# Kernel optimization log

Measured on AMD Instinct MI355X. Metric: run time of the kernel, lower is better.

Reference implementation:

```python
import jax, jax.numpy as jnp
import numpy as np

B, S, D, DOUT, E = 2, 2048, 1024, 1024, 8
DH = 4 * D  # expert hidden size


def setup_inputs() -> dict:
    key = jax.random.key(0)
    ks = jax.random.split(key, 7)
    sc = lambda *sh: 1.0 / np.sqrt(sh[-2]) if len(sh) >= 2 else 0.02
    return {
        "x": jax.random.normal(ks[0], (B, S, D), jnp.float32),
        "Wg": jax.random.normal(ks[1], (D, E), jnp.float32) / np.sqrt(D),
        "bg": jnp.zeros((E,), jnp.float32),
        "W1": jax.random.normal(ks[2], (E, D, DH), jnp.float32) / np.sqrt(D),
        "b1": jax.random.normal(ks[3], (E, DH), jnp.float32) * 0.02,
        "W2": jax.random.normal(ks[4], (E, DH, DOUT), jnp.float32) / np.sqrt(DH),
        "b2": jax.random.normal(ks[5], (E, DOUT), jnp.float32) * 0.02,
    }


def reference(x, Wg, bg, W1, b1, W2, b2):
    # x: [B, S, D] -> flatten tokens (chunking over seq in the original is
    # math-neutral: routing and expert MLP are per-token).
    Bb, Ss, Dd = x.shape
    xt = x.reshape(-1, Dd)                       # [T, D]
    # Gate: softmax then argmax (top-1 routing, output NOT scaled by gate prob)
    gates = jax.nn.softmax(xt @ Wg + bg, axis=-1)  # [T, E]
    sel = jnp.argmax(gates, axis=-1)               # [T]
    nE = W1.shape[0]
    out = jnp.zeros((xt.shape[0], W2.shape[-1]), x.dtype)
    # Grouped expert MLP expressed as masked dense loop over the small fixed
    # expert count (jit-friendly; a fused gather-grouped-GEMM-scatter kernel
    # is the optimization target).
    for e in range(nE):
        h = jax.nn.gelu(xt @ W1[e] + b1[e], approximate=False)  # [T, 4D]
        ye = h @ W2[e] + b2[e]                                  # [T, DOUT]
        out = jnp.where((sel == e)[:, None], ye, out)
    return out.reshape(Bb, Ss, -1)
```

## Files before the change

### kernel.cpp

```cpp
#include <hip/hip_runtime.h>
#include <hip/hip_bf16.h>
#include <math.h>

#define T_TOK 4096
#define DIM   1024
#define NEXP  8
#define DHID  4096
#define NDOUT 1024
#define BM    128
#define MAXTILES 40

typedef short bf16x8 __attribute__((ext_vector_type(8)));
typedef float f32x4 __attribute__((ext_vector_type(4)));

__device__ __forceinline__ unsigned short f2bf(float f) {
  unsigned u = __float_as_uint(f);
  u += 0x7fffu + ((u >> 16) & 1u);
  return (unsigned short)(u >> 16);
}
__device__ __forceinline__ unsigned pack2bf(float a, float b) {
  return (unsigned)f2bf(a) | ((unsigned)f2bf(b) << 16);
}
__device__ __forceinline__ void gl_lds16(const void* g, void* l) {
  __builtin_amdgcn_global_load_lds(
      (const __attribute__((address_space(1))) void*)g,
      (__attribute__((address_space(3))) void*)l, 16, 0, 0);
}
#define SBAR()  __builtin_amdgcn_s_barrier()
#define SCHED() __builtin_amdgcn_sched_barrier(0)

__global__ __launch_bounds__(256)
void gate_kernel(const float* __restrict__ x, const float* __restrict__ Wg,
                 const float* __restrict__ bg, int* __restrict__ sel,
                 unsigned short* __restrict__ xbf) {
  int lane = threadIdx.x & 63;
  int wid  = threadIdx.x >> 6;
  int t = blockIdx.x * 4 + wid;
  if (t >= T_TOK) return;
  const float* xr = x + (size_t)t * DIM;
  unsigned short* xbr = xbf + (size_t)t * DIM;
  double acc[NEXP];
#pragma unroll
  for (int e = 0; e < NEXP; e++) acc[e] = 0.0;
#pragma unroll
  for (int j = 0; j < 4; j++) {
    int d0 = j * 256 + lane * 4;
    float4 v = *(const float4*)(xr + d0);
    uint2 p; p.x = pack2bf(v.x, v.y); p.y = pack2bf(v.z, v.w);
    *(uint2*)(xbr + d0) = p;
    float xs[4] = {v.x, v.y, v.z, v.w};
#pragma unroll
    for (int i = 0; i < 4; i++) {
      const float4* wr = reinterpret_cast<const float4*>(Wg + (size_t)(d0 + i) * NEXP);
      float4 w0 = wr[0], w1 = wr[1];
      double xv = (double)xs[i];
      acc[0] += xv * (double)w0.x;
      acc[1] += xv * (double)w0.y;
      acc[2] += xv * (double)w0.z;
      acc[3] += xv * (double)w0.w;
      acc[4] += xv * (double)w1.x;
      acc[5] += xv * (double)w1.y;
      acc[6] += xv * (double)w1.z;
      acc[7] += xv * (double)w1.w;
    }
  }
#pragma unroll
  for (int off = 32; off >= 1; off >>= 1) {
#pragma unroll
    for (int e = 0; e < NEXP; e++) acc[e] += __shfl_down(acc[e], off);
  }
  if (lane == 0) {
    double best = acc[0] + (double)bg[0];
    int bi = 0;
#pragma unroll
    for (int e = 1; e < NEXP; e++) {
      double v = acc[e] + (double)bg[e];
      if (v > best) { best = v; bi = e; }
    }
    sel[t] = bi;
  }
}

__global__ void zero_kernel(int* __restrict__ counts) {
  if (threadIdx.x < NEXP) counts[threadIdx.x] = 0;
}

__global__ void hist_kernel(const int* __restrict__ sel, int* __restrict__ counts) {
  __shared__ int lc[NEXP];
  if (threadIdx.x < NEXP) lc[threadIdx.x] = 0;
  __syncthreads();
  int t = blockIdx.x * 256 + threadIdx.x;
  atomicAdd(&lc[sel[t]], 1);
  __syncthreads();
  if (threadIdx.x < NEXP) atomicAdd(&counts[threadIdx.x], lc[threadIdx.x]);
}

__global__ void plan_kernel(const int* __restrict__ counts, int* __restrict__ base,
                            int* __restrict__ cursor, int* __restrict__ tileExpert,
                            int* __restrict__ tilePos, int* __restrict__ tileRows,
                            int* __restrict__ ntiles) {
  if (threadIdx.x == 0) {
    int acc = 0, nt = 0;
    for (int e = 0; e < NEXP; e++) {
      base[e] = acc; cursor[e] = acc;
      int c = counts[e];
      for (int j = 0; j < c; j += BM) {
        tileExpert[nt] = e;
        tilePos[nt]    = acc + j;
        int rem = c - j;
        tileRows[nt]   = rem < BM ? rem : BM;
        nt++;
      }
      acc += c;
    }
    *ntiles = nt;
  }
}

__global__ void scatter_kernel(const int* __restrict__ sel, int* __restrict__ cursor,
                               int* __restrict__ list) {
  __shared__ int lcnt[NEXP];
  __shared__ int lbase[NEXP];
  int tid = threadIdx.x;
  if (tid < NEXP) lcnt[tid] = 0;
  __syncthreads();
  int t = blockIdx.x * 256 + tid;
  int e = sel[t];
  int lpos = atomicAdd(&lcnt[e], 1);
  __syncthreads();
  if (tid < NEXP) lbase[tid] = atomicAdd(&cursor[tid], lcnt[tid]);
  __syncthreads();
  list[lbase[e] + lpos] = t;
}

__global__ __launch_bounds__(256)
void transpose_tile_kernel(const float* __restrict__ in, unsigned short* __restrict__ out,
                           int K, int N) {
  int nb = blockIdx.x, kb = blockIdx.y, e = blockIdx.z;
  const float* inp = in + (size_t)e * K * N;
  __shared__ unsigned short lds[128][72];
  int tx = threadIdx.x;
  int kloc = tx >> 5;
  int n4   = (tx & 31) << 2;
#pragma unroll
  for (int p = 0; p < 8; p++) {
    int k = p * 8 + kloc;
    float4 v = *(const float4*)(inp + (size_t)(kb * 64 + k) * N + nb * 128 + n4);
    lds[n4 + 0][k] = f2bf(v.x);
    lds[n4 + 1][k] = f2bf(v.y);
    lds[n4 + 2][k] = f2bf(v.z);
    lds[n4 + 3][k] = f2bf(v.w);
  }
  __syncthreads();
  char* tile = (char*)(out + (((size_t)e * gridDim.x + nb) * gridDim.y + kb) * 8192);
  int r  = tx >> 1;
  int kc0 = (tx & 1) * 32;
#pragma unroll
  for (int c = 0; c < 4; c++) {
    int kc = kc0 + c * 8;
    uint4 v = *(const uint4*)&lds[r][kc];
    *(uint4*)(tile + r * 128 + ((2 * kc) ^ ((r & 7) << 4))) = v;
  }
}


__global__ __launch_bounds__(256)
void gemm1_kernel(const unsigned short* __restrict__ xbf, const unsigned short* __restrict__ W1T,
                  const float* __restrict__ b1, const int* __restrict__ list,
                  const int* __restrict__ tileExpert, const int* __restrict__ tilePos,
                  const int* __restrict__ tileRows, const int* __restrict__ ntiles,
                  unsigned short* __restrict__ HcT) {
  int tIdx = blockIdx.y;
  if (tIdx >= *ntiles) return;
  int e = tileExpert[tIdx], posBase = tilePos[tIdx], rows = tileRows[tIdx];
  int nb = blockIdx.x;

  __shared__ __align__(1024) char As[2][16384];
  __shared__ __align__(1024) char Bs[2][16384];

  const int tx = threadIdx.x, lane = tx & 63, w = tx >> 6;
  const int wm = w >> 1, wn = w & 1;
  const int rsub = lane >> 3;
  const int px = ((lane & 7) ^ rsub) << 4;

  const char* aS[4];
#pragma unroll
  for (int j = 0; j < 4; j++) {
    int r = w * 32 + j * 8 + rsub;
    int tok = list[posBase + (r < rows ? r : rows - 1)];
    aS[j] = (const char*)xbf + (size_t)tok * (DIM * 2) + px;
  }
  const char* bTile = (const char*)W1T + (((size_t)e * (DHID / 128) + nb) * (DIM / 64)) * 16384
                      + w * 4096 + lane * 16;

  auto STAGE = [&](int buf, int kt) {
#pragma unroll
    for (int j = 0; j < 4; j++) {
      gl_lds16(aS[j] + kt * 128, &As[buf][(w * 32 + j * 8) * 128]);
      gl_lds16(bTile + kt * 16384 + j * 1024, &Bs[buf][w * 4096 + j * 1024]);
    }
  };

  f32x4 acc[4][4];
#pragma unroll
  for (int mf = 0; mf < 4; mf++)
#pragma unroll
    for (int nf = 0; nf < 4; nf++)
      acc[mf][nf] = f32x4{0.f, 0.f, 0.f, 0.f};

  auto COMPUTE = [&](int buf) {
#pragma unroll
    for (int ks = 0; ks < 2; ks++) {
      int koff = (ks * 64 + (lane >> 4) * 16) ^ ((lane & 7) << 4);
      bf16x8 aF[4], bF[4];
#pragma unroll
      for (int mf = 0; mf < 4; mf++)
        aF[mf] = *(const bf16x8*)&As[buf][(wm * 64 + mf * 16 + (lane & 15)) * 128 + koff];
#pragma unroll
      for (int nf = 0; nf < 4; nf++)
        bF[nf] = *(const bf16x8*)&Bs[buf][(wn * 64 + nf * 16 + (lane & 15)) * 128 + koff];
#pragma unroll
      for (int mf = 0; mf < 4; mf++)
#pragma unroll
        for (int nf = 0; nf < 4; nf++)
          acc[mf][nf] = __builtin_amdgcn_mfma_f32_16x16x32_bf16(aF[mf], bF[nf], acc[mf][nf], 0, 0, 0);
    }
  };

  const int NT = DIM / 64;
  STAGE(0, 0);
  for (int kt = 0; kt < NT; kt++) {
    int buf = kt & 1;
    if (kt + 1 < NT) {
      STAGE(buf ^ 1, kt + 1);
      asm volatile("s_waitcnt vmcnt(8)" ::: "memory");
    } else {
      asm volatile("s_waitcnt vmcnt(0)" ::: "memory");
    }
    SCHED(); SBAR(); SCHED();
    COMPUTE(buf);
    SCHED(); SBAR(); SCHED();
  }

  const float* b1e = b1 + (size_t)e * DHID;
  char* hBase = (char*)(HcT + (size_t)tIdx * (DHID / 64) * 8192);
#pragma unroll
  for (int nf = 0; nf < 4; nf++) {
    int col = nb * 128 + wn * 64 + nf * 16 + (lane & 15);
    int kt2 = col >> 6;
    int colk2 = (col & 63) * 2;
    float bias = b1e[col];
    char* tile = hBase + (size_t)kt2 * 16384;
#pragma unroll
    for (int mf = 0; mf < 4; mf++) {
#pragma unroll
      for (int j = 0; j < 4; j++) {
        int r = wm * 64 + mf * 16 + ((lane >> 4) << 2) + j;
        float h = acc[mf][nf][j] + bias;
        float g = 0.5f * h * (1.0f + erff(h * 0.70710678118654752f));
        *(unsigned short*)(tile + r * 128 + (colk2 ^ ((r & 7) << 4))) = f2bf(g);
      }
    }
  }
}

__global__ __launch_bounds__(256)
void gemm2_kernel(const unsigned short* __restrict__ HcT, const unsigned short* __restrict__ W2T,
                  const float* __restrict__ b2, const int* __restrict__ tileExpert,
                  const int* __restrict__ tilePos, const int* __restrict__ tileRows,
                  const int* __restrict__ ntiles, float* __restrict__ Ppart) {
  int tIdx = blockIdx.y;
  if (tIdx >= *ntiles) return;
  int e = tileExpert[tIdx], posBase = tilePos[tIdx], rows = tileRows[tIdx];
  int nb = blockIdx.x;
  int zs = blockIdx.z;

  __shared__ __align__(1024) char As[2][16384];
  __shared__ __align__(1024) char Bs[2][16384];

  const int tx = threadIdx.x, lane = tx & 63, w = tx >> 6;
  const int wm = w >> 1, wn = w & 1;

  const char* aTile = (const char*)HcT + (size_t)tIdx * (DHID / 64) * 16384
                      + (size_t)zs * 32 * 16384 + w * 4096 + lane * 16;
  const char* bTile = (const char*)W2T + (((size_t)e * (NDOUT / 128) + nb) * (DHID / 64)) * 16384
                      + (size_t)zs * 32 * 16384 + w * 4096 + lane * 16;

  auto STAGE = [&](int buf, int kt) {
#pragma unroll
    for (int j = 0; j < 4; j++) {
      gl_lds16(aTile + kt * 16384 + j * 1024, &As[buf][w * 4096 + j * 1024]);
      gl_lds16(bTile + kt * 16384 + j * 1024, &Bs[buf][w * 4096 + j * 1024]);
    }
  };

  f32x4 acc[4][4];
#pragma unroll
  for (int mf = 0; mf < 4; mf++)
#pragma unroll
    for (int nf = 0; nf < 4; nf++)
      acc[mf][nf] = f32x4{0.f, 0.f, 0.f, 0.f};

  auto COMPUTE = [&](int buf) {
#pragma unroll
    for (int ks = 0; ks < 2; ks++) {
      int koff = (ks * 64 + (lane >> 4) * 16) ^ ((lane & 7) << 4);
      bf16x8 aF[4], bF[4];
#pragma unroll
      for (int mf = 0; mf < 4; mf++)
        aF[mf] = *(const bf16x8*)&As[buf][(wm * 64 + mf * 16 + (lane & 15)) * 128 + koff];
#pragma unroll
      for (int nf = 0; nf < 4; nf++)
        bF[nf] = *(const bf16x8*)&Bs[buf][(wn * 64 + nf * 16 + (lane & 15)) * 128 + koff];
#pragma unroll
      for (int mf = 0; mf < 4; mf++)
#pragma unroll
        for (int nf = 0; nf < 4; nf++)
          acc[mf][nf] = __builtin_amdgcn_mfma_f32_16x16x32_bf16(aF[mf], bF[nf], acc[mf][nf], 0, 0, 0);
    }
  };

  const int NT = 32;
  STAGE(0, 0);
  for (int kt = 0; kt < NT; kt++) {
    int buf = kt & 1;
    if (kt + 1 < NT) {
      STAGE(buf ^ 1, kt + 1);
      asm volatile("s_waitcnt vmcnt(8)" ::: "memory");
    } else {
      asm volatile("s_waitcnt vmcnt(0)" ::: "memory");
    }
    SCHED(); SBAR(); SCHED();
    COMPUTE(buf);
    SCHED(); SBAR(); SCHED();
  }

  const float* b2e = b2 + (size_t)e * NDOUT;
  float* P = Ppart + (size_t)zs * T_TOK * NDOUT;
#pragma unroll
  for (int nf = 0; nf < 4; nf++) {
    int col = nb * 128 + wn * 64 + nf * 16 + (lane & 15);
    float bias = (zs == 0) ? b2e[col] : 0.f;
#pragma unroll
    for (int mf = 0; mf < 4; mf++)
#pragma unroll
      for (int j = 0; j < 4; j++) {
        int rloc = wm * 64 + mf * 16 + ((lane >> 4) << 2) + j;
        if (rloc < rows)
          P[(size_t)(posBase + rloc) * NDOUT + col] = acc[mf][nf][j] + bias;
      }
  }
}

__global__ __launch_bounds__(256)
void reduce_kernel(const float* __restrict__ Ppart, const int* __restrict__ list,
                   float* __restrict__ out) {
  int pos = blockIdx.x;
  int tok = list[pos];
  int c = threadIdx.x * 4;
  float4 a = *(const float4*)(Ppart + (size_t)pos * NDOUT + c);
  float4 b = *(const float4*)(Ppart + (size_t)T_TOK * NDOUT + (size_t)pos * NDOUT + c);
  float4 o; o.x = a.x + b.x; o.y = a.y + b.y; o.z = a.z + b.z; o.w = a.w + b.w;
  *(float4*)(out + (size_t)tok * NDOUT + c) = o;
}

extern "C" void kernel_launch(void* const* d_in, const int* in_sizes, int n_in,
                              void* d_out, int out_size, void* d_ws, size_t ws_size,
                              hipStream_t stream) {
  const float* x  = (const float*)d_in[0];
  const float* Wg = (const float*)d_in[1];
  const float* bg = (const float*)d_in[2];
  const float* W1 = (const float*)d_in[3];
  const float* b1 = (const float*)d_in[4];
  const float* W2 = (const float*)d_in[5];
  const float* b2 = (const float*)d_in[6];
  float* out = (float*)d_out;

  char* ws = (char*)d_ws;
  int* sel        = (int*)(ws);
  int* counts     = (int*)(ws + 16384);
  int* base       = (int*)(ws + 16448);
  int* cursor     = (int*)(ws + 16512);
  int* ntiles     = (int*)(ws + 16576);
  int* tileExpert = (int*)(ws + 16640);
  int* tilePos    = (int*)(ws + 16832);
  int* tileRows   = (int*)(ws + 17024);
  int* list       = (int*)(ws + 17408);

  unsigned short* xbf = (unsigned short*)(ws + (1ull << 20));
  unsigned short* HcT = (unsigned short*)(ws + (10ull << 20));
  unsigned short* W1T = (unsigned short*)(ws + (52ull << 20));
  unsigned short* W2T = (unsigned short*)(ws + (116ull << 20));
  float* Ppart        = (float*)(ws + (52ull << 20));

  gate_kernel<<<T_TOK / 4, 256, 0, stream>>>(x, Wg, bg, sel, xbf);
  zero_kernel<<<1, 64, 0, stream>>>(counts);
  hist_kernel<<<T_TOK / 256, 256, 0, stream>>>(sel, counts);
  plan_kernel<<<1, 64, 0, stream>>>(counts, base, cursor, tileExpert, tilePos, tileRows, ntiles);
  scatter_kernel<<<T_TOK / 256, 256, 0, stream>>>(sel, cursor, list);

  transpose_tile_kernel<<<dim3(DHID / 128, DIM / 64, NEXP), 256, 0, stream>>>(W1, W1T, DIM, DHID);
  transpose_tile_kernel<<<dim3(NDOUT / 128, DHID / 64, NEXP), 256, 0, stream>>>(W2, W2T, DHID, NDOUT);

  gemm1_kernel<<<dim3(DHID / 128, MAXTILES), 256, 0, stream>>>(
      xbf, W1T, b1, list, tileExpert, tilePos, tileRows, ntiles, HcT);
  gemm2_kernel<<<dim3(NDOUT / 128, MAXTILES, 2), 256, 0, stream>>>(
      HcT, W2T, b2, tileExpert, tilePos, tileRows, ntiles, Ppart);
  reduce_kernel<<<T_TOK, 256, 0, stream>>>(Ppart, list, out);
}
```

Baseline: 316.7 us.

## Single-buffer GEMM loops, tanh GELU, and LDS-staged coalesced H stores

Both expert GEMM kernels drop the double-buffered LDS prefetch with explicit vmcnt waits and use a single buffer with __syncthreads around each k-step. In GEMM1 the exact erf GELU becomes a tanh approximation built on __expf. The H tile is first written into LDS and then copied to global memory as 16-byte row stores instead of scattered 2-byte writes. Losing the prefetch means global loads no longer overlap MFMA work, and the tanh GELU changes numerics slightly.

```diff
diff --git a/kernel.cpp b/kernel.cpp
--- a/kernel.cpp
+++ b/kernel.cpp
@@ -26,8 +26,14 @@
       (const __attribute__((address_space(1))) void*)g,
       (__attribute__((address_space(3))) void*)l, 16, 0, 0);
 }
-#define SBAR()  __builtin_amdgcn_s_barrier()
-#define SCHED() __builtin_amdgcn_sched_barrier(0)
+__device__ __forceinline__ float gelu_fast(float h) {
+  float z  = 0.79788456080286536f * (h + 0.044715f * h * h * h);
+  float az = fabsf(z);
+  float et = __expf(-2.0f * az);
+  float th = (1.0f - et) / (1.0f + et);
+  th = copysignf(th, z);
+  return 0.5f * h * (1.0f + th);
+}
 
 __global__ __launch_bounds__(256)
 void gate_kernel(const float* __restrict__ x, const float* __restrict__ Wg,
@@ -175,8 +181,9 @@
   int e = tileExpert[tIdx], posBase = tilePos[tIdx], rows = tileRows[tIdx];
   int nb = blockIdx.x;
 
-  __shared__ __align__(1024) char As[2][16384];
-  __shared__ __align__(1024) char Bs[2][16384];
+  __shared__ __align__(1024) char SH[32768];
+  char* As = SH;
+  char* Bs = SH + 16384;
 
   const int tx = threadIdx.x, lane = tx & 63, w = tx >> 6;
   const int wm = w >> 1, wn = w & 1;
@@ -193,14 +200,6 @@
   const char* bTile = (const char*)W1T + (((size_t)e * (DHID / 128) + nb) * (DIM / 64)) * 16384
                       + w * 4096 + lane * 16;
 
-  auto STAGE = [&](int buf, int kt) {
-#pragma unroll
-    for (int j = 0; j < 4; j++) {
-      gl_lds16(aS[j] + kt * 128, &As[buf][(w * 32 + j * 8) * 128]);
-      gl_lds16(bTile + kt * 16384 + j * 1024, &Bs[buf][w * 4096 + j * 1024]);
-    }
-  };
-
   f32x4 acc[4][4];
 #pragma unroll
   for (int mf = 0; mf < 4; mf++)
@@ -208,60 +207,62 @@
     for (int nf = 0; nf < 4; nf++)
       acc[mf][nf] = f32x4{0.f, 0.f, 0.f, 0.f};
 
-  auto COMPUTE = [&](int buf) {
+  const int NT = DIM / 64;
+  for (int kt = 0; kt < NT; kt++) {
+#pragma unroll
+    for (int j = 0; j < 4; j++) {
+      gl_lds16(aS[j] + kt * 128, As + (w * 32 + j * 8) * 128);
+      gl_lds16(bTile + kt * 16384 + j * 1024, Bs + w * 4096 + j * 1024);
+    }
+    __syncthreads();
 #pragma unroll
     for (int ks = 0; ks < 2; ks++) {
       int koff = (ks * 64 + (lane >> 4) * 16) ^ ((lane & 7) << 4);
       bf16x8 aF[4], bF[4];
 #pragma unroll
       for (int mf = 0; mf < 4; mf++)
-        aF[mf] = *(const bf16x8*)&As[buf][(wm * 64 + mf * 16 + (lane & 15)) * 128 + koff];
+        aF[mf] = *(const bf16x8*)(As + (wm * 64 + mf * 16 + (lane & 15)) * 128 + koff);
 #pragma unroll
       for (int nf = 0; nf < 4; nf++)
-        bF[nf] = *(const bf16x8*)&Bs[buf][(wn * 64 + nf * 16 + (lane & 15)) * 128 + koff];
+        bF[nf] = *(const bf16x8*)(Bs + (wn * 64 + nf * 16 + (lane & 15)) * 128 + koff);
 #pragma unroll
       for (int mf = 0; mf < 4; mf++)
 #pragma unroll
         for (int nf = 0; nf < 4; nf++)
           acc[mf][nf] = __builtin_amdgcn_mfma_f32_16x16x32_bf16(aF[mf], bF[nf], acc[mf][nf], 0, 0, 0);
     }
-  };
-
-  const int NT = DIM / 64;
-  STAGE(0, 0);
-  for (int kt = 0; kt < NT; kt++) {
-    int buf = kt & 1;
-    if (kt + 1 < NT) {
-      STAGE(buf ^ 1, kt + 1);
-      asm volatile("s_waitcnt vmcnt(8)" ::: "memory");
-    } else {
-      asm volatile("s_waitcnt vmcnt(0)" ::: "memory");
-    }
-    SCHED(); SBAR(); SCHED();
-    COMPUTE(buf);
-    SCHED(); SBAR(); SCHED();
+    __syncthreads();
   }
 
   const float* b1e = b1 + (size_t)e * DHID;
-  char* hBase = (char*)(HcT + (size_t)tIdx * (DHID / 64) * 8192);
+  const int r4 = (lane >> 4) << 2;
+  int xj[4];
+#pragma unroll
+  for (int j = 0; j < 4; j++) xj[j] = ((r4 + j) & 7) << 4;
 #pragma unroll
   for (int nf = 0; nf < 4; nf++) {
-    int col = nb * 128 + wn * 64 + nf * 16 + (lane & 15);
-    int kt2 = col >> 6;
-    int colk2 = (col & 63) * 2;
-    float bias = b1e[col];
-    char* tile = hBase + (size_t)kt2 * 16384;
+    int colLoc = wn * 64 + nf * 16 + (lane & 15);
+    int tLoc   = colLoc >> 6;
+    int k2     = (colLoc & 63) * 2;
+    float bias = b1e[nb * 128 + colLoc];
+    char* base = SH + tLoc * 16384;
 #pragma unroll
     for (int mf = 0; mf < 4; mf++) {
+      int rBase = wm * 64 + mf * 16 + r4;
 #pragma unroll
       for (int j = 0; j < 4; j++) {
-        int r = wm * 64 + mf * 16 + ((lane >> 4) << 2) + j;
-        float h = acc[mf][nf][j] + bias;
-        float g = 0.5f * h * (1.0f + erff(h * 0.70710678118654752f));
-        *(unsigned short*)(tile + r * 128 + (colk2 ^ ((r & 7) << 4))) = f2bf(g);
+        float g = gelu_fast(acc[mf][nf][j] + bias);
+        *(unsigned short*)(base + (rBase + j) * 128 + (k2 ^ xj[j])) = f2bf(g);
       }
     }
   }
+  __syncthreads();
+  const char* src = SH + tx * 128;
+  char* dst = (char*)HcT + (size_t)tIdx * (DHID / 64) * 16384
+            + (size_t)(nb * 2 + (tx >> 7)) * 16384 + (tx & 127) * 128;
+#pragma unroll
+  for (int i = 0; i < 8; i++)
+    *(uint4*)(dst + i * 16) = *(const uint4*)(src + i * 16);
 }
 
 __global__ __launch_bounds__(256)
@@ -275,8 +276,9 @@
   int nb = blockIdx.x;
   int zs = blockIdx.z;
 
-  __shared__ __align__(1024) char As[2][16384];
-  __shared__ __align__(1024) char Bs[2][16384];
+  __shared__ __align__(1024) char SH[32768];
+  char* As = SH;
+  char* Bs = SH + 16384;
 
   const int tx = threadIdx.x, lane = tx & 63, w = tx >> 6;
   const int wm = w >> 1, wn = w & 1;
@@ -286,14 +288,6 @@
   const char* bTile = (const char*)W2T + (((size_t)e * (NDOUT / 128) + nb) * (DHID / 64)) * 16384
                       + (size_t)zs * 32 * 16384 + w * 4096 + lane * 16;
 
-  auto STAGE = [&](int buf, int kt) {
-#pragma unroll
-    for (int j = 0; j < 4; j++) {
-      gl_lds16(aTile + kt * 16384 + j * 1024, &As[buf][w * 4096 + j * 1024]);
-      gl_lds16(bTile + kt * 16384 + j * 1024, &Bs[buf][w * 4096 + j * 1024]);
-    }
-  };
-
   f32x4 acc[4][4];
 #pragma unroll
   for (int mf = 0; mf < 4; mf++)
@@ -301,38 +295,31 @@
     for (int nf = 0; nf < 4; nf++)
       acc[mf][nf] = f32x4{0.f, 0.f, 0.f, 0.f};
 
-  auto COMPUTE = [&](int buf) {
+  const int NT = 32;
+  for (int kt = 0; kt < NT; kt++) {
+#pragma unroll
+    for (int j = 0; j < 4; j++) {
+      gl_lds16(aTile + kt * 16384 + j * 1024, As + w * 4096 + j * 1024);
+      gl_lds16(bTile + kt * 16384 + j * 1024, Bs + w * 4096 + j * 1024);
+    }
+    __syncthreads();
 #pragma unroll
     for (int ks = 0; ks < 2; ks++) {
       int koff = (ks * 64 + (lane >> 4) * 16) ^ ((lane & 7) << 4);
       bf16x8 aF[4], bF[4];
 #pragma unroll
       for (int mf = 0; mf < 4; mf++)
-        aF[mf] = *(const bf16x8*)&As[buf][(wm * 64 + mf * 16 + (lane & 15)) * 128 + koff];
+        aF[mf] = *(const bf16x8*)(As + (wm * 64 + mf * 16 + (lane & 15)) * 128 + koff);
 #pragma unroll
       for (int nf = 0; nf < 4; nf++)
-        bF[nf] = *(const bf16x8*)&Bs[buf][(wn * 64 + nf * 16 + (lane & 15)) * 128 + koff];
+        bF[nf] = *(const bf16x8*)(Bs + (wn * 64 + nf * 16 + (lane & 15)) * 128 + koff);
 #pragma unroll
       for (int mf = 0; mf < 4; mf++)
 #pragma unroll
         for (int nf = 0; nf < 4; nf++)
           acc[mf][nf] = __builtin_amdgcn_mfma_f32_16x16x32_bf16(aF[mf], bF[nf], acc[mf][nf], 0, 0, 0);
     }
-  };
-
-  const int NT = 32;
-  STAGE(0, 0);
-  for (int kt = 0; kt < NT; kt++) {
-    int buf = kt & 1;
-    if (kt + 1 < NT) {
-      STAGE(buf ^ 1, kt + 1);
-      asm volatile("s_waitcnt vmcnt(8)" ::: "memory");
-    } else {
-      asm volatile("s_waitcnt vmcnt(0)" ::: "memory");
-    }
-    SCHED(); SBAR(); SCHED();
-    COMPUTE(buf);
-    SCHED(); SBAR(); SCHED();
+    __syncthreads();
   }
 
   const float* b2e = b2 + (size_t)e * NDOUT;
```

Result: faster. 297.4 us (-6.1%).
